# Kernel optimization log

Hardware: AMD Instinct MI355X
Metric: run time of the kernel (lower is better)

Reference implementation:

```python
import jax, jax.numpy as jnp
import numpy as np

B, D, DP, H = 65536, 512, 256, 8
HD = D // H  # head dim = 64
EPS = 1e-5


def _layernorm(x, gamma, beta):
    mu = jnp.mean(x, axis=-1, keepdims=True)
    var = jnp.var(x, axis=-1, keepdims=True)
    return (x - mu) * jax.lax.rsqrt(var + EPS) * gamma + beta


def setup_inputs() -> dict:
    key = jax.random.key(0)
    ks = jax.random.split(key, 16)
    n = lambda k, shape, s=0.02: (jax.random.normal(k, shape, jnp.float32) * s)
    return {
        "cell_emb": jax.random.normal(ks[0], (B, D), jnp.float32),
        "pert_emb": jax.random.normal(ks[1], (B, DP), jnp.float32),
        # perturbation_proj: Linear(DP -> D)
        "Wp": n(ks[2], (D, DP)), "bp": jnp.zeros((D,), jnp.float32),
        # MultiheadAttention in/out projections (each D x D)
        "Wq": n(ks[3], (D, D)), "bq": jnp.zeros((D,), jnp.float32),
        "Wk": n(ks[4], (D, D)), "bk": jnp.zeros((D,), jnp.float32),
        "Wv": n(ks[5], (D, D)), "bv": jnp.zeros((D,), jnp.float32),
        "Wo": n(ks[6], (D, D)), "bo": jnp.zeros((D,), jnp.float32),
        # norm1, norm2
        "g1": jnp.ones((D,), jnp.float32), "be1": jnp.zeros((D,), jnp.float32),
        "g2": jnp.ones((D,), jnp.float32), "be2": jnp.zeros((D,), jnp.float32),
        # FFN: Linear(D -> 2D), GELU, Linear(2D -> D)
        "W1": n(ks[7], (2 * D, D)), "b1": jnp.zeros((2 * D,), jnp.float32),
        "W2": n(ks[8], (D, 2 * D)), "b2": jnp.zeros((D,), jnp.float32),
    }


def reference(cell_emb, pert_emb, Wp, bp, Wq, bq, Wk, bk, Wv, bv, Wo, bo,
              g1, be1, g2, be2, W1, b1, W2, b2):
    # kv = perturbation_proj(pert_emb), length-1 KV sequence
    kv = pert_emb @ Wp.T + bp                       # (B, D)
    # MultiheadAttention with q_len = kv_len = 1
    q = (cell_emb @ Wq.T + bq).reshape(B, H, HD)    # (B, H, HD)
    k = (kv @ Wk.T + bk).reshape(B, H, HD)
    v = (kv @ Wv.T + bv).reshape(B, H, HD)
    # scores over a single key -> softmax yields 1, kept for faithfulness
    logits = jnp.sum(q * k, axis=-1, keepdims=True) / jnp.sqrt(jnp.float32(HD))  # (B, H, 1)
    w = jax.nn.softmax(logits, axis=-1)             # == ones (single key)
    attn = (w * v).reshape(B, D)
    attn_out = attn @ Wo.T + bo                     # (B, D)
    x = _layernorm(cell_emb + attn_out, g1, be1)
    # FFN with exact (erf) GELU, matching torch nn.GELU default
    h = jax.nn.gelu(x @ W1.T + b1, approximate=False)
    ffn_out = h @ W2.T + b2
    return _layernorm(x + ffn_out, g2, be2)
```

## Files before the change

kernel.cpp:

```cpp
#include <hip/hip_runtime.h>
#include <hip/hip_bf16.h>

typedef __bf16 bf16_t;
typedef __attribute__((ext_vector_type(8))) __bf16 bf16x8;
typedef __attribute__((ext_vector_type(4))) float f32x4;


__global__ __launch_bounds__(256) void prep_wvp_fast(
    const float* __restrict__ Wv, const float* __restrict__ Wp,
    const float* __restrict__ bp, const float* __restrict__ bv,
    float* __restrict__ Wvp, float* __restrict__ bvp) {
  const int t = threadIdx.x;
  const int rs = t >> 6;
  const int jg = t & 63;
  const int i = blockIdx.x * 4 + rs;
  const float* wrow = Wv + (size_t)i * 512;
  float4 acc = {0.f, 0.f, 0.f, 0.f};
#pragma unroll 4
  for (int d = 0; d < 512; ++d) {
    const float s = wrow[d];
    const float4 p = *(const float4*)&Wp[d * 256 + jg * 4];
    acc.x += s * p.x; acc.y += s * p.y; acc.z += s * p.z; acc.w += s * p.w;
  }
  *(float4*)&Wvp[(size_t)i * 256 + jg * 4] = acc;
  float pb = 0.f;
#pragma unroll
  for (int u = 0; u < 8; ++u) { const int d = jg * 8 + u; pb += wrow[d] * bp[d]; }
#pragma unroll
  for (int m = 1; m <= 32; m <<= 1) pb += __shfl_xor(pb, m);
  if (jg == 0) bvp[i] = pb + bv[i];
}

__global__ __launch_bounds__(256) void prep_wc_cast(
    const float* __restrict__ Wo, const float* __restrict__ bo,
    const float* __restrict__ Wvp, const float* __restrict__ bvp,
    bf16_t* __restrict__ Wc, float* __restrict__ bcomb,
    const float* __restrict__ W1, const float* __restrict__ W2,
    bf16_t* __restrict__ W1b, bf16_t* __restrict__ W2b) {
  const int b = blockIdx.x;
  const int t = threadIdx.x;
  if (b < 128) {
    const int rs = t >> 6, jg = t & 63;
    const int o = b * 4 + rs;
    const float* worow = Wo + (size_t)o * 512;
    float4 acc = {0.f, 0.f, 0.f, 0.f};
#pragma unroll 4
    for (int i = 0; i < 512; ++i) {
      const float s = worow[i];
      const float4 p = *(const float4*)&Wvp[i * 256 + jg * 4];
      acc.x += s * p.x; acc.y += s * p.y; acc.z += s * p.z; acc.w += s * p.w;
    }
    const int g = o >> 4, rr = o & 15;
    const float av[4] = {acc.x, acc.y, acc.z, acc.w};
#pragma unroll
    for (int u = 0; u < 4; ++u) {
      const int k = jg * 4 + u;
      const int tt = k >> 5, q = (k >> 3) & 3, e = k & 7;
      Wc[((((size_t)g * 8 + tt) * 64) + q * 16 + rr) * 8 + e] = (bf16_t)av[u];
    }
    float pb = 0.f;
#pragma unroll
    for (int u = 0; u < 8; ++u) { const int i = jg * 8 + u; pb += worow[i] * bvp[i]; }
#pragma unroll
    for (int m = 1; m <= 32; m <<= 1) pb += __shfl_xor(pb, m);
    if (jg == 0) bcomb[o] = pb + bo[o];
  } else {
    const int idx = ((b - 128) * 256 + t) * 8;
    const float* s;
    bf16_t* d;
    if (idx < 524288) {
      const int o = idx >> 9, k = idx & 511;
      const int g = o >> 4, rr = o & 15, tt = k >> 5, q = (k >> 3) & 3;
      s = W1 + idx;
      d = W1b + ((((size_t)g * 16 + tt) * 64) + q * 16 + rr) * 8;
    } else {
      const int i2 = idx - 524288;
      const int o = i2 >> 10, k = i2 & 1023;
      const int g = o >> 4, rr = o & 15, tt = k >> 5, q = (k >> 3) & 3;
      s = W2 + i2;
      d = W2b + ((((size_t)g * 32 + tt) * 64) + q * 16 + rr) * 8;
    }
    float4 u0 = *(const float4*)s;
    float4 u1 = *(const float4*)(s + 4);
    bf16x8 v;
    v[0] = (bf16_t)u0.x; v[1] = (bf16_t)u0.y; v[2] = (bf16_t)u0.z; v[3] = (bf16_t)u0.w;
    v[4] = (bf16_t)u1.x; v[5] = (bf16_t)u1.y; v[6] = (bf16_t)u1.z; v[7] = (bf16_t)u1.w;
    *(bf16x8*)d = v;
  }
}


__device__ __forceinline__ int alay(int row, int k) {
  const int rr = row & 15;
  const int c = (k >> 3) & 3;
  return ((k >> 5) * 2 + (row >> 4)) * 512 +
         (rr * 4 + (c ^ ((rr >> 1) & 3))) * 8 + (k & 7);
}

template <int STEPS, int NJ>
__device__ __forceinline__ void kloop(const bf16_t* __restrict__ lA_,
                                      const bf16_t* __restrict__ Bp,
                                      int g0, int SB, int soff,
                                      int fRd, int lane,
                                      f32x4 (&acc)[2][NJ]) {
  auto bfrag = [&](int j, int s) {
    return *(const bf16x8*)(Bp + ((size_t)((g0 + j) * SB + (soff + s)) * 64 + lane) * 8);
  };
  auto afrag = [&](int i, int s) {
    return *(const bf16x8*)&lA_[(s * 2 + i) * 512 + fRd];
  };
  bf16x8 bCur[NJ], bNxt[NJ], aCur[2], aNxt[2];
#pragma unroll
  for (int j = 0; j < NJ; ++j) bCur[j] = bfrag(j, 0);
#pragma unroll
  for (int i = 0; i < 2; ++i) aCur[i] = afrag(i, 0);
#pragma unroll
  for (int s = 0; s < STEPS; ++s) {
    if (s + 1 < STEPS) {
#pragma unroll
      for (int j = 0; j < NJ; ++j) bNxt[j] = bfrag(j, s + 1);
#pragma unroll
      for (int i = 0; i < 2; ++i) aNxt[i] = afrag(i, s + 1);
    }
    __builtin_amdgcn_s_setprio(1);
#pragma unroll
    for (int j = 0; j < NJ; ++j)
#pragma unroll
      for (int i = 0; i < 2; ++i)
        acc[i][j] = __builtin_amdgcn_mfma_f32_16x16x32_bf16(aCur[i], bCur[j], acc[i][j], 0, 0, 0);
    __builtin_amdgcn_s_setprio(0);
#pragma unroll
    for (int j = 0; j < NJ; ++j) bCur[j] = bNxt[j];
#pragma unroll
    for (int i = 0; i < 2; ++i) aCur[i] = aNxt[i];
  }
}

__global__ __launch_bounds__(256, 2) void fused_block(
    const float* __restrict__ pert, const bf16_t* __restrict__ Wc,
    const float* __restrict__ bcomb, const float* __restrict__ cell,
    const float* __restrict__ g1, const float* __restrict__ be1,
    const bf16_t* __restrict__ W1b, const float* __restrict__ b1,
    const bf16_t* __restrict__ W2b, const float* __restrict__ b2,
    const float* __restrict__ g2, const float* __restrict__ be2,
    float* __restrict__ out) {

  __shared__ __align__(16) bf16_t lX[32 * 512];
  __shared__ __align__(16) bf16_t lH[32 * 256];
  float* rsP = (float*)lH;
  float* ssP = (float*)lH + 128;

  const int t = threadIdx.x;
  const int m0 = blockIdx.x * 32;
  const int lane = t & 63;
  const int wc = t >> 6;
  const int r = lane & 15;
  const int q = lane >> 4;
  const int qs = q ^ ((r >> 1) & 3);
  const int fRd = r * 32 + qs * 8;

#pragma unroll
  for (int u = 0; u < 4; ++u) {
    const int g = u * 256 + t;
    const int row = g >> 5;
    const int c = g & 31;
    const float* src = pert + (size_t)(m0 + row) * 256 + c * 8;
    float4 u0 = *(const float4*)src;
    float4 u1 = *(const float4*)(src + 4);
    bf16x8 v;
    v[0] = (bf16_t)u0.x; v[1] = (bf16_t)u0.y; v[2] = (bf16_t)u0.z; v[3] = (bf16_t)u0.w;
    v[4] = (bf16_t)u1.x; v[5] = (bf16_t)u1.y; v[6] = (bf16_t)u1.z; v[7] = (bf16_t)u1.w;
    *(bf16x8*)&lH[alay(row, c * 8)] = v;
  }
  __syncthreads();

  {
    f32x4 acc1[2][8];
#pragma unroll
    for (int i = 0; i < 2; ++i)
#pragma unroll
      for (int j = 0; j < 8; ++j)
#pragma unroll
        for (int p = 0; p < 4; ++p) acc1[i][j][p] = 0.f;
    kloop<8, 8>(lH, Wc, 8 * wc, 8, 0, fRd, lane, acc1);

    float s_[2][4], ss_[2][4];
#pragma unroll
    for (int i = 0; i < 2; ++i)
#pragma unroll
      for (int p = 0; p < 4; ++p) { s_[i][p] = 0.f; ss_[i][p] = 0.f; }
    float bb[8];
#pragma unroll
    for (int j = 0; j < 8; ++j) bb[j] = bcomb[128 * wc + 16 * j + r];
#pragma unroll
    for (int i = 0; i < 2; ++i)
#pragma unroll
      for (int p = 0; p < 4; ++p) {
        const int rowl = 16 * i + 4 * q + p;
#pragma unroll
        for (int j = 0; j < 8; ++j) {
          const int col = 128 * wc + 16 * j + r;
          float v = acc1[i][j][p] + bb[j] + cell[(size_t)(m0 + rowl) * 512 + col];
          acc1[i][j][p] = v;
          s_[i][p] += v;
          ss_[i][p] += v * v;
        }
      }
#pragma unroll
    for (int m = 1; m <= 8; m <<= 1)
#pragma unroll
      for (int i = 0; i < 2; ++i)
#pragma unroll
        for (int p = 0; p < 4; ++p) {
          s_[i][p] += __shfl_xor(s_[i][p], m);
          ss_[i][p] += __shfl_xor(ss_[i][p], m);
        }
    __syncthreads();
    if (r == 0) {
#pragma unroll
      for (int i = 0; i < 2; ++i)
#pragma unroll
        for (int p = 0; p < 4; ++p) {
          const int rowl = 16 * i + 4 * q + p;
          rsP[wc * 32 + rowl] = s_[i][p];
          ssP[wc * 32 + rowl] = ss_[i][p];
        }
    }
    __syncthreads();
    float mu[2][4], inv[2][4];
#pragma unroll
    for (int i = 0; i < 2; ++i)
#pragma unroll
      for (int p = 0; p < 4; ++p) {
        const int rowl = 16 * i + 4 * q + p;
        float tS = rsP[rowl] + rsP[32 + rowl] + rsP[64 + rowl] + rsP[96 + rowl];
        float tQ = ssP[rowl] + ssP[32 + rowl] + ssP[64 + rowl] + ssP[96 + rowl];
        float m_ = tS * (1.0f / 512.0f);
        float v_ = tQ * (1.0f / 512.0f) - m_ * m_;
        mu[i][p] = m_;
        inv[i][p] = rsqrtf(v_ + 1e-5f);
      }
    float ga[8], be[8];
#pragma unroll
    for (int j = 0; j < 8; ++j) {
      ga[j] = g1[128 * wc + 16 * j + r];
      be[j] = be1[128 * wc + 16 * j + r];
    }
#pragma unroll
    for (int i = 0; i < 2; ++i)
#pragma unroll
      for (int p = 0; p < 4; ++p) {
        const int rowl = 16 * i + 4 * q + p;
#pragma unroll
        for (int j = 0; j < 8; ++j) {
          const int col = 128 * wc + 16 * j + r;
          float v = (acc1[i][j][p] - mu[i][p]) * inv[i][p] * ga[j] + be[j];
          lX[alay(rowl, col)] = (bf16_t)v;
        }
      }
  }
  __syncthreads();

  f32x4 acc3[2][8];
#pragma unroll
  for (int i = 0; i < 2; ++i)
#pragma unroll
    for (int j = 0; j < 8; ++j)
#pragma unroll
      for (int p = 0; p < 4; ++p) acc3[i][j][p] = 0.f;

  for (int qh = 0; qh < 4; ++qh) {
    {
      f32x4 accq[2][4];
#pragma unroll
      for (int i = 0; i < 2; ++i)
#pragma unroll
        for (int j = 0; j < 4; ++j)
#pragma unroll
          for (int p = 0; p < 4; ++p) accq[i][j][p] = 0.f;
      kloop<16, 4>(lX, W1b, 16 * qh + 4 * wc, 16, 0, fRd, lane, accq);
      float bb1[4];
#pragma unroll
      for (int j = 0; j < 4; ++j) bb1[j] = b1[256 * qh + 64 * wc + 16 * j + r];
#pragma unroll
      for (int i = 0; i < 2; ++i)
#pragma unroll
        for (int p = 0; p < 4; ++p) {
          const int rowl = 16 * i + 4 * q + p;
#pragma unroll
          for (int j = 0; j < 4; ++j) {
            const int col = 64 * wc + 16 * j + r;
            float v = accq[i][j][p] + bb1[j];
            float g = 0.5f * v * (1.0f + erff(v * 0.70710678118654752f));
            lH[alay(rowl, col)] = (bf16_t)g;
          }
        }
    }
    __syncthreads();
    kloop<8, 8>(lH, W2b, 8 * wc, 32, 8 * qh, fRd, lane, acc3);
    __syncthreads();
  }

  {
    float s_[2][4], ss_[2][4];
#pragma unroll
    for (int i = 0; i < 2; ++i)
#pragma unroll
      for (int p = 0; p < 4; ++p) { s_[i][p] = 0.f; ss_[i][p] = 0.f; }
    float bb2[8];
#pragma unroll
    for (int j = 0; j < 8; ++j) bb2[j] = b2[128 * wc + 16 * j + r];
#pragma unroll
    for (int i = 0; i < 2; ++i)
#pragma unroll
      for (int p = 0; p < 4; ++p) {
        const int rowl = 16 * i + 4 * q + p;
#pragma unroll
        for (int j = 0; j < 8; ++j) {
          const int col = 128 * wc + 16 * j + r;
          float v = acc3[i][j][p] + bb2[j] + (float)lX[alay(rowl, col)];
          acc3[i][j][p] = v;
          s_[i][p] += v;
          ss_[i][p] += v * v;
        }
      }
#pragma unroll
    for (int m = 1; m <= 8; m <<= 1)
#pragma unroll
      for (int i = 0; i < 2; ++i)
#pragma unroll
        for (int p = 0; p < 4; ++p) {
          s_[i][p] += __shfl_xor(s_[i][p], m);
          ss_[i][p] += __shfl_xor(ss_[i][p], m);
        }
    if (r == 0) {
#pragma unroll
      for (int i = 0; i < 2; ++i)
#pragma unroll
        for (int p = 0; p < 4; ++p) {
          const int rowl = 16 * i + 4 * q + p;
          rsP[wc * 32 + rowl] = s_[i][p];
          ssP[wc * 32 + rowl] = ss_[i][p];
        }
    }
    __syncthreads();
    float mu[2][4], inv[2][4];
#pragma unroll
    for (int i = 0; i < 2; ++i)
#pragma unroll
      for (int p = 0; p < 4; ++p) {
        const int rowl = 16 * i + 4 * q + p;
        float tS = rsP[rowl] + rsP[32 + rowl] + rsP[64 + rowl] + rsP[96 + rowl];
        float tQ = ssP[rowl] + ssP[32 + rowl] + ssP[64 + rowl] + ssP[96 + rowl];
        float m_ = tS * (1.0f / 512.0f);
        float v_ = tQ * (1.0f / 512.0f) - m_ * m_;
        mu[i][p] = m_;
        inv[i][p] = rsqrtf(v_ + 1e-5f);
      }
    float ga[8], be[8];
#pragma unroll
    for (int j = 0; j < 8; ++j) {
      ga[j] = g2[128 * wc + 16 * j + r];
      be[j] = be2[128 * wc + 16 * j + r];
    }
#pragma unroll
    for (int i = 0; i < 2; ++i)
#pragma unroll
      for (int p = 0; p < 4; ++p) {
        const int rowl = 16 * i + 4 * q + p;
#pragma unroll
        for (int j = 0; j < 8; ++j) {
          const int col = 128 * wc + 16 * j + r;
          out[(size_t)(m0 + rowl) * 512 + col] =
              (acc3[i][j][p] - mu[i][p]) * inv[i][p] * ga[j] + be[j];
        }
      }
  }
}

extern "C" void kernel_launch(void* const* d_in, const int* in_sizes, int n_in,
                              void* d_out, int out_size, void* d_ws, size_t ws_size,
                              hipStream_t stream) {
  const float* cell = (const float*)d_in[0];
  const float* pert = (const float*)d_in[1];
  const float* Wp   = (const float*)d_in[2];
  const float* bp   = (const float*)d_in[3];
  const float* Wv   = (const float*)d_in[8];
  const float* bv   = (const float*)d_in[9];
  const float* Wo   = (const float*)d_in[10];
  const float* bo   = (const float*)d_in[11];
  const float* g1   = (const float*)d_in[12];
  const float* be1  = (const float*)d_in[13];
  const float* g2   = (const float*)d_in[14];
  const float* be2  = (const float*)d_in[15];
  const float* W1   = (const float*)d_in[16];
  const float* b1   = (const float*)d_in[17];
  const float* W2   = (const float*)d_in[18];
  const float* b2   = (const float*)d_in[19];

  char* ws = (char*)d_ws;
  float*  Wvp   = (float*)(ws + 0);
  float*  bvp   = (float*)(ws + 524288);
  float*  bcomb = (float*)(ws + 526336);
  bf16_t* Wc    = (bf16_t*)(ws + 528384);
  bf16_t* W1b   = (bf16_t*)(ws + 790528);
  bf16_t* W2b   = (bf16_t*)(ws + 1839104);
  (void)in_sizes; (void)n_in; (void)out_size; (void)ws_size;

  prep_wvp_fast<<<128, 256, 0, stream>>>(Wv, Wp, bp, bv, Wvp, bvp);
  prep_wc_cast<<<640, 256, 0, stream>>>(Wo, bo, Wvp, bvp, Wc, bcomb,
                                        W1, W2, W1b, W2b);

  fused_block<<<2048, 256, 0, stream>>>(pert, Wc, bcomb, cell, g1, be1,
                                        W1b, b1, W2b, b2, g2, be2,
                                        (float*)d_out);
}
```

Baseline: 598.9 us.

## Split fused block across 8 waves, restructure MFMA k-loop, polynomial GELU

Doubles the block to 512 threads so each of 8 waves owns half as many output columns, halving per-wave accumulators and raising occupancy via launch bounds (512,4). The k-loop now issues MFMAs on half of the B fragments while the other half loads, and drops A-fragment double-buffering. The pert staging moves to lX, and the LayerNorm partial-sum buffers grow to hold 8 waves. erff is replaced by an Abramowitz-Stegun polynomial with __expf. This risks slightly lower GELU accuracy and more cross-wave reductions and B-fragment reloads per wave.

```diff
diff --git a/kernel.cpp b/kernel.cpp
--- a/kernel.cpp
+++ b/kernel.cpp
@@ -4,7 +4,6 @@
 typedef __bf16 bf16_t;
 typedef __attribute__((ext_vector_type(8))) __bf16 bf16x8;
 typedef __attribute__((ext_vector_type(4))) float f32x4;
-
 
 __global__ __launch_bounds__(256) void prep_wvp_fast(
     const float* __restrict__ Wv, const float* __restrict__ Wp,
@@ -97,46 +96,59 @@
          (rr * 4 + (c ^ ((rr >> 1) & 3))) * 8 + (k & 7);
 }
 
+__device__ __forceinline__ float gelu_exact(float v) {
+  const float u = v * 0.70710678118654752f;
+  const float xa = fabsf(u);
+  const float tt = 1.0f / (1.0f + 0.3275911f * xa);
+  const float poly = ((((1.061405429f * tt - 1.453152027f) * tt + 1.421413741f) * tt
+                       - 0.284496736f) * tt + 0.254829592f) * tt;
+  const float y = 1.0f - poly * __expf(-xa * xa);
+  const float er = (u < 0.f) ? -y : y;
+  return 0.5f * v * (1.0f + er);
+}
+
 template <int STEPS, int NJ>
 __device__ __forceinline__ void kloop(const bf16_t* __restrict__ lA_,
                                       const bf16_t* __restrict__ Bp,
                                       int g0, int SB, int soff,
                                       int fRd, int lane,
                                       f32x4 (&acc)[2][NJ]) {
+  constexpr int H = NJ / 2;
   auto bfrag = [&](int j, int s) {
     return *(const bf16x8*)(Bp + ((size_t)((g0 + j) * SB + (soff + s)) * 64 + lane) * 8);
   };
-  auto afrag = [&](int i, int s) {
-    return *(const bf16x8*)&lA_[(s * 2 + i) * 512 + fRd];
-  };
-  bf16x8 bCur[NJ], bNxt[NJ], aCur[2], aNxt[2];
-#pragma unroll
-  for (int j = 0; j < NJ; ++j) bCur[j] = bfrag(j, 0);
-#pragma unroll
-  for (int i = 0; i < 2; ++i) aCur[i] = afrag(i, 0);
+  bf16x8 bA[H], bB[H];
+#pragma unroll
+  for (int j = 0; j < H; ++j) bA[j] = bfrag(j, 0);
 #pragma unroll
   for (int s = 0; s < STEPS; ++s) {
+#pragma unroll
+    for (int j = 0; j < H; ++j) bB[j] = bfrag(H + j, s);
+    bf16x8 af[2];
+#pragma unroll
+    for (int i = 0; i < 2; ++i) af[i] = *(const bf16x8*)&lA_[(s * 2 + i) * 512 + fRd];
+    __builtin_amdgcn_s_setprio(1);
+#pragma unroll
+    for (int j = 0; j < H; ++j)
+#pragma unroll
+      for (int i = 0; i < 2; ++i)
+        acc[i][j] = __builtin_amdgcn_mfma_f32_16x16x32_bf16(af[i], bA[j], acc[i][j], 0, 0, 0);
+    __builtin_amdgcn_s_setprio(0);
     if (s + 1 < STEPS) {
 #pragma unroll
-      for (int j = 0; j < NJ; ++j) bNxt[j] = bfrag(j, s + 1);
-#pragma unroll
-      for (int i = 0; i < 2; ++i) aNxt[i] = afrag(i, s + 1);
+      for (int j = 0; j < H; ++j) bA[j] = bfrag(j, s + 1);
     }
     __builtin_amdgcn_s_setprio(1);
 #pragma unroll
-    for (int j = 0; j < NJ; ++j)
-#pragma unroll
-      for (int i = 0; i < 2; ++i)
-        acc[i][j] = __builtin_amdgcn_mfma_f32_16x16x32_bf16(aCur[i], bCur[j], acc[i][j], 0, 0, 0);
+    for (int j = 0; j < H; ++j)
+#pragma unroll
+      for (int i = 0; i < 2; ++i)
+        acc[i][H + j] = __builtin_amdgcn_mfma_f32_16x16x32_bf16(af[i], bB[j], acc[i][H + j], 0, 0, 0);
     __builtin_amdgcn_s_setprio(0);
-#pragma unroll
-    for (int j = 0; j < NJ; ++j) bCur[j] = bNxt[j];
-#pragma unroll
-    for (int i = 0; i < 2; ++i) aCur[i] = aNxt[i];
-  }
-}
-
-__global__ __launch_bounds__(256, 2) void fused_block(
+  }
+}
+
+__global__ __launch_bounds__(512, 4) void fused_block(
     const float* __restrict__ pert, const bf16_t* __restrict__ Wc,
     const float* __restrict__ bcomb, const float* __restrict__ cell,
     const float* __restrict__ g1, const float* __restrict__ be1,
@@ -148,7 +160,7 @@
   __shared__ __align__(16) bf16_t lX[32 * 512];
   __shared__ __align__(16) bf16_t lH[32 * 256];
   float* rsP = (float*)lH;
-  float* ssP = (float*)lH + 128;
+  float* ssP = (float*)lH + 256;
 
   const int t = threadIdx.x;
   const int m0 = blockIdx.x * 32;
@@ -160,8 +172,8 @@
   const int fRd = r * 32 + qs * 8;
 
 #pragma unroll
-  for (int u = 0; u < 4; ++u) {
-    const int g = u * 256 + t;
+  for (int u = 0; u < 2; ++u) {
+    const int g = u * 512 + t;
     const int row = g >> 5;
     const int c = g & 31;
     const float* src = pert + (size_t)(m0 + row) * 256 + c * 8;
@@ -170,36 +182,36 @@
     bf16x8 v;
     v[0] = (bf16_t)u0.x; v[1] = (bf16_t)u0.y; v[2] = (bf16_t)u0.z; v[3] = (bf16_t)u0.w;
     v[4] = (bf16_t)u1.x; v[5] = (bf16_t)u1.y; v[6] = (bf16_t)u1.z; v[7] = (bf16_t)u1.w;
-    *(bf16x8*)&lH[alay(row, c * 8)] = v;
+    *(bf16x8*)&lX[alay(row, c * 8)] = v;
   }
   __syncthreads();
 
   {
-    f32x4 acc1[2][8];
-#pragma unroll
-    for (int i = 0; i < 2; ++i)
-#pragma unroll
-      for (int j = 0; j < 8; ++j)
+    f32x4 acc1[2][4];
+#pragma unroll
+    for (int i = 0; i < 2; ++i)
+#pragma unroll
+      for (int j = 0; j < 4; ++j)
 #pragma unroll
         for (int p = 0; p < 4; ++p) acc1[i][j][p] = 0.f;
-    kloop<8, 8>(lH, Wc, 8 * wc, 8, 0, fRd, lane, acc1);
+    kloop<8, 4>(lX, Wc, 4 * wc, 8, 0, fRd, lane, acc1);
 
     float s_[2][4], ss_[2][4];
 #pragma unroll
     for (int i = 0; i < 2; ++i)
 #pragma unroll
       for (int p = 0; p < 4; ++p) { s_[i][p] = 0.f; ss_[i][p] = 0.f; }
-    float bb[8];
-#pragma unroll
-    for (int j = 0; j < 8; ++j) bb[j] = bcomb[128 * wc + 16 * j + r];
-#pragma unroll
-    for (int i = 0; i < 2; ++i)
-#pragma unroll
-      for (int p = 0; p < 4; ++p) {
-        const int rowl = 16 * i + 4 * q + p;
-#pragma unroll
-        for (int j = 0; j < 8; ++j) {
-          const int col = 128 * wc + 16 * j + r;
+    float bb[4];
+#pragma unroll
+    for (int j = 0; j < 4; ++j) bb[j] = bcomb[64 * wc + 16 * j + r];
+#pragma unroll
+    for (int i = 0; i < 2; ++i)
+#pragma unroll
+      for (int p = 0; p < 4; ++p) {
+        const int rowl = 16 * i + 4 * q + p;
+#pragma unroll
+        for (int j = 0; j < 4; ++j) {
+          const int col = 64 * wc + 16 * j + r;
           float v = acc1[i][j][p] + bb[j] + cell[(size_t)(m0 + rowl) * 512 + col];
           acc1[i][j][p] = v;
           s_[i][p] += v;
@@ -233,27 +245,28 @@
 #pragma unroll
       for (int p = 0; p < 4; ++p) {
         const int rowl = 16 * i + 4 * q + p;
-        float tS = rsP[rowl] + rsP[32 + rowl] + rsP[64 + rowl] + rsP[96 + rowl];
-        float tQ = ssP[rowl] + ssP[32 + rowl] + ssP[64 + rowl] + ssP[96 + rowl];
+        float tS = 0.f, tQ = 0.f;
+#pragma unroll
+        for (int w2 = 0; w2 < 8; ++w2) { tS += rsP[w2 * 32 + rowl]; tQ += ssP[w2 * 32 + rowl]; }
         float m_ = tS * (1.0f / 512.0f);
         float v_ = tQ * (1.0f / 512.0f) - m_ * m_;
         mu[i][p] = m_;
         inv[i][p] = rsqrtf(v_ + 1e-5f);
       }
-    float ga[8], be[8];
-#pragma unroll
-    for (int j = 0; j < 8; ++j) {
-      ga[j] = g1[128 * wc + 16 * j + r];
-      be[j] = be1[128 * wc + 16 * j + r];
-    }
-#pragma unroll
-    for (int i = 0; i < 2; ++i)
-#pragma unroll
-      for (int p = 0; p < 4; ++p) {
-        const int rowl = 16 * i + 4 * q + p;
-#pragma unroll
-        for (int j = 0; j < 8; ++j) {
-          const int col = 128 * wc + 16 * j + r;
+    float ga[4], be[4];
+#pragma unroll
+    for (int j = 0; j < 4; ++j) {
+      ga[j] = g1[64 * wc + 16 * j + r];
+      be[j] = be1[64 * wc + 16 * j + r];
+    }
+#pragma unroll
+    for (int i = 0; i < 2; ++i)
+#pragma unroll
+      for (int p = 0; p < 4; ++p) {
+        const int rowl = 16 * i + 4 * q + p;
+#pragma unroll
+        for (int j = 0; j < 4; ++j) {
+          const int col = 64 * wc + 16 * j + r;
           float v = (acc1[i][j][p] - mu[i][p]) * inv[i][p] * ga[j] + be[j];
           lX[alay(rowl, col)] = (bf16_t)v;
         }
@@ -261,43 +274,41 @@
   }
   __syncthreads();
 
-  f32x4 acc3[2][8];
+  f32x4 acc3[2][4];
 #pragma unroll
   for (int i = 0; i < 2; ++i)
 #pragma unroll
-    for (int j = 0; j < 8; ++j)
+    for (int j = 0; j < 4; ++j)
 #pragma unroll
       for (int p = 0; p < 4; ++p) acc3[i][j][p] = 0.f;
 
   for (int qh = 0; qh < 4; ++qh) {
     {
-      f32x4 accq[2][4];
-#pragma unroll
-      for (int i = 0; i < 2; ++i)
-#pragma unroll
-        for (int j = 0; j < 4; ++j)
+      f32x4 accq[2][2];
+#pragma unroll
+      for (int i = 0; i < 2; ++i)
+#pragma unroll
+        for (int j = 0; j < 2; ++j)
 #pragma unroll
           for (int p = 0; p < 4; ++p) accq[i][j][p] = 0.f;
-      kloop<16, 4>(lX, W1b, 16 * qh + 4 * wc, 16, 0, fRd, lane, accq);
-      float bb1[4];
-#pragma unroll
-      for (int j = 0; j < 4; ++j) bb1[j] = b1[256 * qh + 64 * wc + 16 * j + r];
+      kloop<16, 2>(lX, W1b, 16 * qh + 2 * wc, 16, 0, fRd, lane, accq);
+      float bb1[2];
+#pragma unroll
+      for (int j = 0; j < 2; ++j) bb1[j] = b1[256 * qh + 32 * wc + 16 * j + r];
 #pragma unroll
       for (int i = 0; i < 2; ++i)
 #pragma unroll
         for (int p = 0; p < 4; ++p) {
           const int rowl = 16 * i + 4 * q + p;
 #pragma unroll
-          for (int j = 0; j < 4; ++j) {
-            const int col = 64 * wc + 16 * j + r;
-            float v = accq[i][j][p] + bb1[j];
-            float g = 0.5f * v * (1.0f + erff(v * 0.70710678118654752f));
-            lH[alay(rowl, col)] = (bf16_t)g;
+          for (int j = 0; j < 2; ++j) {
+            const int col = 32 * wc + 16 * j + r;
+            lH[alay(rowl, col)] = (bf16_t)gelu_exact(accq[i][j][p] + bb1[j]);
           }
         }
     }
     __syncthreads();
-    kloop<8, 8>(lH, W2b, 8 * wc, 32, 8 * qh, fRd, lane, acc3);
+    kloop<8, 4>(lH, W2b, 4 * wc, 32, 8 * qh, fRd, lane, acc3);
     __syncthreads();
   }
 
@@ -307,17 +318,17 @@
     for (int i = 0; i < 2; ++i)
 #pragma unroll
       for (int p = 0; p < 4; ++p) { s_[i][p] = 0.f; ss_[i][p] = 0.f; }
-    float bb2[8];
-#pragma unroll
-    for (int j = 0; j < 8; ++j) bb2[j] = b2[128 * wc + 16 * j + r];
-#pragma unroll
-    for (int i = 0; i < 2; ++i)
-#pragma unroll
-      for (int p = 0; p < 4; ++p) {
-        const int rowl = 16 * i + 4 * q + p;
-#pragma unroll
-        for (int j = 0; j < 8; ++j) {
-          const int col = 128 * wc + 16 * j + r;
+    float bb2[4];
+#pragma unroll
+    for (int j = 0; j < 4; ++j) bb2[j] = b2[64 * wc + 16 * j + r];
+#pragma unroll
+    for (int i = 0; i < 2; ++i)
+#pragma unroll
+      for (int p = 0; p < 4; ++p) {
+        const int rowl = 16 * i + 4 * q + p;
+#pragma unroll
+        for (int j = 0; j < 4; ++j) {
+          const int col = 64 * wc + 16 * j + r;
           float v = acc3[i][j][p] + bb2[j] + (float)lX[alay(rowl, col)];
           acc3[i][j][p] = v;
           s_[i][p] += v;
@@ -350,27 +361,28 @@
 #pragma unroll
       for (int p = 0; p < 4; ++p) {
         const int rowl = 16 * i + 4 * q + p;
-        float tS = rsP[rowl] + rsP[32 + rowl] + rsP[64 + rowl] + rsP[96 + rowl];
-        float tQ = ssP[rowl] + ssP[32 + rowl] + ssP[64 + rowl] + ssP[96 + rowl];
+        float tS = 0.f, tQ = 0.f;
+#pragma unroll
+        for (int w2 = 0; w2 < 8; ++w2) { tS += rsP[w2 * 32 + rowl]; tQ += ssP[w2 * 32 + rowl]; }
         float m_ = tS * (1.0f / 512.0f);
         float v_ = tQ * (1.0f / 512.0f) - m_ * m_;
         mu[i][p] = m_;
         inv[i][p] = rsqrtf(v_ + 1e-5f);
       }
-    float ga[8], be[8];
-#pragma unroll
-    for (int j = 0; j < 8; ++j) {
-      ga[j] = g2[128 * wc + 16 * j + r];
-      be[j] = be2[128 * wc + 16 * j + r];
-    }
-#pragma unroll
-    for (int i = 0; i < 2; ++i)
-#pragma unroll
-      for (int p = 0; p < 4; ++p) {
-        const int rowl = 16 * i + 4 * q + p;
-#pragma unroll
-        for (int j = 0; j < 8; ++j) {
-          const int col = 128 * wc + 16 * j + r;
+    float ga[4], be[4];
+#pragma unroll
+    for (int j = 0; j < 4; ++j) {
+      ga[j] = g2[64 * wc + 16 * j + r];
+      be[j] = be2[64 * wc + 16 * j + r];
+    }
+#pragma unroll
+    for (int i = 0; i < 2; ++i)
+#pragma unroll
+      for (int p = 0; p < 4; ++p) {
+        const int rowl = 16 * i + 4 * q + p;
+#pragma unroll
+        for (int j = 0; j < 4; ++j) {
+          const int col = 64 * wc + 16 * j + r;
           out[(size_t)(m0 + rowl) * 512 + col] =
               (acc3[i][j][p] - mu[i][p]) * inv[i][p] * ga[j] + be[j];
         }
@@ -411,7 +423,7 @@
   prep_wc_cast<<<640, 256, 0, stream>>>(Wo, bo, Wvp, bvp, Wc, bcomb,
                                         W1, W2, W1b, W2b);
 
-  fused_block<<<2048, 256, 0, stream>>>(pert, Wc, bcomb, cell, g1, be1,
+  fused_block<<<2048, 512, 0, stream>>>(pert, Wc, bcomb, cell, g1, be1,
                                         W1b, b1, W2b, b2, g2, be2,
                                         (float*)d_out);
 }
```

After: 623.0 us. +4.0%, slower.
